# Optimization experiments

Hardware: AMD Instinct MI355X
Metric: run time of the kernel (lower is better)

## Reference

```python
import jax, jax.numpy as jnp
import numpy as np

CHUNK = 32  # chunk_size in _delta_rule_chunkwise

def _l2norm(x, eps=1e-6):
    return x * jax.lax.rsqrt(jnp.sum(x * x, axis=-1, keepdims=True) + eps)

def setup_inputs() -> dict:
    key = jax.random.key(0)
    kq, kk, kv, kb = jax.random.split(key, 4)
    b, h, L, dk, dv = 2, 8, 4096, 128, 128
    return {
        "q": jax.random.normal(kq, (b, h, L, dk), jnp.float32),
        "k": jax.random.normal(kk, (b, h, L, dk), jnp.float32),
        "v": jax.random.normal(kv, (b, h, L, dv), jnp.float32),
        "beta": jax.random.uniform(kb, (b, h, L), jnp.float32),  # sigmoid(b_proj) in (0,1)
    }

def _delta_rule_chunkwise(q, k, v, beta, chunk_size=CHUNK):
    b, h, L, dk = q.shape
    dv = v.shape[-1]
    c = chunk_size
    pad = (-L) % c
    if pad:
        q = jnp.pad(q, ((0, 0), (0, 0), (0, pad), (0, 0)))
        k = jnp.pad(k, ((0, 0), (0, 0), (0, pad), (0, 0)))
        v = jnp.pad(v, ((0, 0), (0, 0), (0, pad), (0, 0)))
        beta = jnp.pad(beta, ((0, 0), (0, 0), (0, pad)))
    n = (L + pad) // c
    q = _l2norm(q)
    k = _l2norm(k)
    v = v * beta[..., None]
    k_beta = k * beta[..., None]
    # [b,h,n,c,d]
    resh = lambda t: t.reshape(b, h, n, c, t.shape[-1])
    q, k, v, k_beta = map(resh, (q, k, v, k_beta))
    # strictly-lower-triangular -(k_beta k^T)
    lower = jnp.tril(jnp.ones((c, c), bool), -1)
    att = -(k_beta @ jnp.swapaxes(k, -1, -2)) * lower
    # forward substitution: invert (I - A) for strictly lower A (unrolled, c=32 static)
    for i in range(1, c):
        upd = jnp.einsum('...j,...jm->...m', att[..., i, :], att[..., :, :i])
        att = att.at[..., i, :i].add(upd)
    att = att + jnp.eye(c, dtype=att.dtype)
    att = att.astype(jnp.bfloat16).astype(q.dtype)  # matches .to(torch.bfloat16)
    u = att @ v         # [b,h,n,c,dv]
    w = att @ k_beta    # [b,h,n,c,dk]
    future = jnp.triu(jnp.ones((c, c), bool), 1)
    S0 = jnp.zeros((b, h, dk, dv), q.dtype)

    def step(S, inp):
        q_i, k_i, u_i, w_i = inp  # [b,h,c,d]
        att_local = jnp.where(future, 0.0, q_i @ jnp.swapaxes(k_i, -1, -2))
        u_new = u_i - w_i @ S
        o_i = q_i @ S + att_local @ u_new
        S_new = S + jnp.swapaxes(k_i, -1, -2) @ u_new
        return S_new, o_i

    xs = tuple(jnp.moveaxis(t, 2, 0) for t in (q, k, u, w))  # scan over chunks
    S, o = jax.lax.scan(step, S0, xs)
    o = jnp.moveaxis(o, 0, 2).reshape(b, h, n * c, dv)[:, :, :L]
    return o, S

def reference(q, k, v, beta):
    return _delta_rule_chunkwise(q, k, v, beta)
```

## Files before the change

kernel.cpp:

```cpp
#include <hip/hip_runtime.h>
#include <hip/hip_bf16.h>


#define B 2
#define H 8
#define LSEQ 4096
#define DK 128
#define DV 128
#define C 32
#define NCHUNK (LSEQ / C)
#define BH (B * H)
#define NBLK (BH * NCHUNK)

typedef _Float16 f16x8 __attribute__((ext_vector_type(8)));
typedef float f32x4 __attribute__((ext_vector_type(4)));

union U4H8 { uint4 u; f16x8 h; };

__device__ inline unsigned short f2h(float f) {
    _Float16 h = (_Float16)f;
    unsigned short u;
    __builtin_memcpy(&u, &h, 2);
    return u;
}
__device__ inline float h2f(unsigned int v) {
    unsigned short s = (unsigned short)v;
    _Float16 h;
    __builtin_memcpy(&h, &s, 2);
    return (float)h;
}
__device__ inline unsigned int pack2(float a, float b) {
    return (unsigned int)f2h(a) | ((unsigned int)f2h(b) << 16);
}
__device__ inline float dot4(float4 a, float4 b) {
    return a.x * b.x + a.y * b.y + a.z * b.z + a.w * b.w;
}
__device__ inline float bf16r(float x) {
    return __bfloat162float(__float2bfloat16(x));
}
__device__ inline uint2 pk4(float v0, float v1, float v2, float v3) {
    uint2 p; p.x = pack2(v0, v1); p.y = pack2(v2, v3); return p;
}

#define S40 40
#define S136 136

__global__ __launch_bounds__(64) void phase2_kernel(
    const float* __restrict__ qg, const float* __restrict__ kg,
    const float* __restrict__ vg, const float* __restrict__ betag,
    uint4* __restrict__ wnegf, uint4* __restrict__ qnf,
    uint4* __restrict__ ktf, uint4* __restrict__ atf,
    uint2* __restrict__ uf)
{
    __shared__ alignas(16) _Float16 sA [32 * S40];
    __shared__ alignas(16) _Float16 sAT[32 * S40];
    __shared__ alignas(16) _Float16 sTT[32 * S40];
    __shared__ alignas(16) _Float16 sTB[32 * S40];
    __shared__ alignas(16) _Float16 sW [32 * S136];
    __shared__ alignas(16) float sbetaL[32];
    __shared__ alignas(16) float skscL[32];

    const int l = threadIdx.x;
    const int lm = l & 15, qd = l >> 4;
    const int blk = blockIdx.x;
    const long tb = (long)blk * C * DK;
    const f32x4 z4 = {0.f, 0.f, 0.f, 0.f};

    if (l < 32) sbetaL[l] = betag[(long)blk * C + l];

    U4H8 qF[8], kF[8];
    float ssq[2] = {0.f, 0.f}, ssk[2] = {0.f, 0.f};
    #pragma unroll
    for (int mt = 0; mt < 2; mt++) {
        #pragma unroll
        for (int kt = 0; kt < 4; kt++) {
            const float* qp = qg + tb + (long)(mt * 16 + lm) * DK + kt * 32 + qd * 8;
            const float* kp = kg + tb + (long)(mt * 16 + lm) * DK + kt * 32 + qd * 8;
            float4 a0 = *(const float4*)qp, a1 = *(const float4*)(qp + 4);
            float4 b0 = *(const float4*)kp, b1 = *(const float4*)(kp + 4);
            ssq[mt] += dot4(a0, a0) + dot4(a1, a1);
            ssk[mt] += dot4(b0, b0) + dot4(b1, b1);
            U4H8 x;
            x.u.x = pack2(a0.x, a0.y); x.u.y = pack2(a0.z, a0.w);
            x.u.z = pack2(a1.x, a1.y); x.u.w = pack2(a1.z, a1.w);
            qF[mt * 4 + kt] = x;
            U4H8 y;
            y.u.x = pack2(b0.x, b0.y); y.u.y = pack2(b0.z, b0.w);
            y.u.z = pack2(b1.x, b1.y); y.u.w = pack2(b1.z, b1.w);
            kF[mt * 4 + kt] = y;
        }
    }
    float qsc[2], ksc[2];
    #pragma unroll
    for (int mt = 0; mt < 2; mt++) {
        float s = ssq[mt];
        s += __shfl_xor(s, 16, 64);
        s += __shfl_xor(s, 32, 64);
        qsc[mt] = rsqrtf(s + 1e-6f);
        float t = ssk[mt];
        t += __shfl_xor(t, 16, 64);
        t += __shfl_xor(t, 32, 64);
        ksc[mt] = rsqrtf(t + 1e-6f);
    }
    if (qd == 0) { skscL[lm] = ksc[0]; skscL[16 + lm] = ksc[1]; }

    f32x4 alT[3] = {z4, z4, z4};
    #pragma unroll
    for (int kt = 0; kt < 4; kt++) {
        alT[0] = __builtin_amdgcn_mfma_f32_16x16x32_f16(kF[kt].h,     qF[kt].h,     alT[0], 0, 0, 0);
        alT[1] = __builtin_amdgcn_mfma_f32_16x16x32_f16(kF[kt].h,     qF[4 + kt].h, alT[1], 0, 0, 0);
        alT[2] = __builtin_amdgcn_mfma_f32_16x16x32_f16(kF[4 + kt].h, qF[4 + kt].h, alT[2], 0, 0, 0);
    }
    #pragma unroll
    for (int mt = 0; mt < 2; mt++) {
        _Float16 qs = (_Float16)qsc[mt];
        #pragma unroll
        for (int kt = 0; kt < 4; kt++) {
            U4H8 x;
            x.h = qF[mt * 4 + kt].h * qs;
            qnf[((long)blk * 8 + mt * 4 + kt) * 64 + l] = x.u;
        }
    }
    f32x4 rw[4] = {z4, z4, z4, z4};
    #pragma unroll
    for (int kt = 0; kt < 4; kt++) {
        rw[0] = __builtin_amdgcn_mfma_f32_16x16x32_f16(kF[kt].h,     kF[kt].h,     rw[0], 0, 0, 0);
        rw[1] = __builtin_amdgcn_mfma_f32_16x16x32_f16(kF[kt].h,     kF[4 + kt].h, rw[1], 0, 0, 0);
        rw[2] = __builtin_amdgcn_mfma_f32_16x16x32_f16(kF[4 + kt].h, kF[kt].h,     rw[2], 0, 0, 0);
        rw[3] = __builtin_amdgcn_mfma_f32_16x16x32_f16(kF[4 + kt].h, kF[4 + kt].h, rw[3], 0, 0, 0);
    }

    float4 b4[2], ks4[2];
    b4[0]  = *(const float4*)&sbetaL[qd * 4];      b4[1]  = *(const float4*)&sbetaL[16 + qd * 4];
    ks4[0] = *(const float4*)&skscL[qd * 4];       ks4[1] = *(const float4*)&skscL[16 + qd * 4];
    const float bcol0 = sbetaL[lm], bcol1 = sbetaL[16 + lm];
    const float bA4[2] = {(&b4[0].x)[0], 0.f}; (void)bA4;

    {
        *(uint2*)&sTB[lm * S40 + 16 + qd * 4] = (uint2){0u, 0u};
        float v[4];
        #pragma unroll
        for (int r = 0; r < 4; r++) {
            int c = qd * 4 + r;
            v[r] = (c <= lm) ? (qsc[0] * (&ks4[0].x)[r] * alT[0][r]) : 0.f;
        }
        *(uint2*)&sTB[lm * S40 + qd * 4] = pk4(v[0], v[1], v[2], v[3]);
        #pragma unroll
        for (int r = 0; r < 4; r++) v[r] = qsc[1] * (&ks4[0].x)[r] * alT[1][r];
        *(uint2*)&sTB[(16 + lm) * S40 + qd * 4] = pk4(v[0], v[1], v[2], v[3]);
        #pragma unroll
        for (int r = 0; r < 4; r++) {
            int c = qd * 4 + r;
            v[r] = (c <= lm) ? (qsc[1] * (&ks4[1].x)[r] * alT[2][r]) : 0.f;
        }
        *(uint2*)&sTB[(16 + lm) * S40 + 16 + qd * 4] = pk4(v[0], v[1], v[2], v[3]);
    }
    #pragma unroll
    for (int f = 0; f < 2; f++) {
        uint4 x = *(const uint4*)&sTB[(f * 16 + lm) * S40 + qd * 8];
        atf[((long)blk * 2 + f) * 64 + l] = x;
    }

    {
        float v[4];
        *(uint2*)&sA [lm * S40 + 16 + qd * 4]        = (uint2){0u, 0u};
        *(uint2*)&sAT[(16 + lm) * S40 + qd * 4]      = (uint2){0u, 0u};
        *(uint2*)&sTT[(16 + lm) * S40 + qd * 4]      = (uint2){0u, 0u};
        #pragma unroll
        for (int r = 0; r < 4; r++) {
            int c = qd * 4 + r;
            v[r] = (c < lm) ? (-bcol0 * ksc[0] * (&ks4[0].x)[r] * rw[0][r]) : 0.f;
        }
        *(uint2*)&sA[lm * S40 + qd * 4] = pk4(v[0], v[1], v[2], v[3]);
        #pragma unroll
        for (int r = 0; r < 4; r++) v[r] = -bcol1 * ksc[1] * (&ks4[0].x)[r] * rw[1][r];
        *(uint2*)&sA[(16 + lm) * S40 + qd * 4] = pk4(v[0], v[1], v[2], v[3]);
        #pragma unroll
        for (int r = 0; r < 4; r++) {
            int c = qd * 4 + r;
            v[r] = (c < lm) ? (-bcol1 * ksc[1] * (&ks4[1].x)[r] * rw[3][r]) : 0.f;
        }
        *(uint2*)&sA[(16 + lm) * S40 + 16 + qd * 4] = pk4(v[0], v[1], v[2], v[3]);
        #pragma unroll
        for (int r = 0; r < 4; r++) {
            int c = qd * 4 + r;
            v[r] = (c > lm) ? (-(&b4[0].x)[r] * (&ks4[0].x)[r] * ksc[0] * rw[0][r]) : 0.f;
        }
        *(uint2*)&sAT[lm * S40 + qd * 4] = pk4(v[0], v[1], v[2], v[3]);
        #pragma unroll
        for (int r = 0; r < 4; r++) v[r] = -(&b4[1].x)[r] * (&ks4[1].x)[r] * ksc[0] * rw[2][r];
        *(uint2*)&sAT[lm * S40 + 16 + qd * 4] = pk4(v[0], v[1], v[2], v[3]);
        #pragma unroll
        for (int r = 0; r < 4; r++) {
            int c = qd * 4 + r;
            v[r] = (c > lm) ? (-(&b4[1].x)[r] * (&ks4[1].x)[r] * ksc[1] * rw[3][r]) : 0.f;
        }
        *(uint2*)&sAT[(16 + lm) * S40 + 16 + qd * 4] = pk4(v[0], v[1], v[2], v[3]);
        #pragma unroll
        for (int r = 0; r < 4; r++) {
            int c = qd * 4 + r;
            v[r] = (c > lm) ? (-(&b4[0].x)[r] * (&ks4[0].x)[r] * ksc[0] * rw[0][r])
                            : ((c == lm) ? 1.0f : 0.f);
        }
        *(uint2*)&sTT[lm * S40 + qd * 4] = pk4(v[0], v[1], v[2], v[3]);
        #pragma unroll
        for (int r = 0; r < 4; r++) v[r] = -(&b4[1].x)[r] * (&ks4[1].x)[r] * ksc[0] * rw[2][r];
        *(uint2*)&sTT[lm * S40 + 16 + qd * 4] = pk4(v[0], v[1], v[2], v[3]);
        #pragma unroll
        for (int r = 0; r < 4; r++) {
            int c = qd * 4 + r;
            v[r] = (c > lm) ? (-(&b4[1].x)[r] * (&ks4[1].x)[r] * ksc[1] * rw[3][r])
                            : ((c == lm) ? 1.0f : 0.f);
        }
        *(uint2*)&sTT[(16 + lm) * S40 + 16 + qd * 4] = pk4(v[0], v[1], v[2], v[3]);
    }
    f32x4 Tc[3], TTc[3];
    #pragma unroll
    for (int r = 0; r < 4; r++) {
        int rr = qd * 4 + r;
        Tc[0][r] = (lm < rr) ? (-(&b4[0].x)[r] * (&ks4[0].x)[r] * ksc[0] * rw[0][r])
                             : ((lm == rr) ? 1.0f : 0.f);
        Tc[1][r] = -(&b4[1].x)[r] * (&ks4[1].x)[r] * ksc[0] * rw[2][r];
        Tc[2][r] = (lm < rr) ? (-(&b4[1].x)[r] * (&ks4[1].x)[r] * ksc[1] * rw[3][r])
                             : ((lm == rr) ? 1.0f : 0.f);
        TTc[0][r] = (rr < lm) ? (-bcol0 * ksc[0] * (&ks4[0].x)[r] * rw[0][r])
                              : ((rr == lm) ? 1.0f : 0.f);
        TTc[1][r] = -bcol1 * ksc[1] * (&ks4[0].x)[r] * rw[1][r];
        TTc[2][r] = (rr < lm) ? (-bcol1 * ksc[1] * (&ks4[1].x)[r] * rw[3][r])
                              : ((rr == lm) ? 1.0f : 0.f);
    }

    #pragma unroll
    for (int p = 0; p < 4; p++) {
        U4H8 AF[2], ATF[2], TTF[2];
        AF[0].u  = *(const uint4*)&sA [lm * S40 + qd * 8];
        AF[1].u  = *(const uint4*)&sA [(16 + lm) * S40 + qd * 8];
        ATF[0].u = *(const uint4*)&sAT[lm * S40 + qd * 8];
        ATF[1].u = *(const uint4*)&sAT[(16 + lm) * S40 + qd * 8];
        TTF[0].u = *(const uint4*)&sTT[lm * S40 + qd * 8];
        TTF[1].u = *(const uint4*)&sTT[(16 + lm) * S40 + qd * 8];

        f32x4 A2_00 = __builtin_amdgcn_mfma_f32_16x16x32_f16(AF[0].h, ATF[0].h, z4, 0, 0, 0);
        f32x4 A2_10 = __builtin_amdgcn_mfma_f32_16x16x32_f16(AF[1].h, ATF[0].h, z4, 0, 0, 0);
        f32x4 A2_11 = __builtin_amdgcn_mfma_f32_16x16x32_f16(AF[1].h, ATF[1].h, z4, 0, 0, 0);
        f32x4 A2T_00 = __builtin_amdgcn_mfma_f32_16x16x32_f16(ATF[0].h, AF[0].h, z4, 0, 0, 0);
        f32x4 A2T_01 = __builtin_amdgcn_mfma_f32_16x16x32_f16(ATF[0].h, AF[1].h, z4, 0, 0, 0);
        f32x4 A2T_11 = __builtin_amdgcn_mfma_f32_16x16x32_f16(ATF[1].h, AF[1].h, z4, 0, 0, 0);

        {
            float v[4];
            #pragma unroll
            for (int r = 0; r < 4; r++) { int c = qd * 4 + r; v[r] = (c < lm) ? A2T_00[r] : 0.f; }
            *(uint2*)&sA[lm * S40 + qd * 4] = pk4(v[0], v[1], v[2], v[3]);
            *(uint2*)&sA[(16 + lm) * S40 + qd * 4] = pk4(A2T_01[0], A2T_01[1], A2T_01[2], A2T_01[3]);
            #pragma unroll
            for (int r = 0; r < 4; r++) { int c = qd * 4 + r; v[r] = (c < lm) ? A2T_11[r] : 0.f; }
            *(uint2*)&sA[(16 + lm) * S40 + 16 + qd * 4] = pk4(v[0], v[1], v[2], v[3]);
        }
        if (p < 3) {
            float v[4];
            #pragma unroll
            for (int r = 0; r < 4; r++) { int c = qd * 4 + r; v[r] = (c > lm) ? A2_00[r] : 0.f; }
            *(uint2*)&sAT[lm * S40 + qd * 4] = pk4(v[0], v[1], v[2], v[3]);
            *(uint2*)&sAT[lm * S40 + 16 + qd * 4] = pk4(A2_10[0], A2_10[1], A2_10[2], A2_10[3]);
            #pragma unroll
            for (int r = 0; r < 4; r++) { int c = qd * 4 + r; v[r] = (c > lm) ? A2_11[r] : 0.f; }
            *(uint2*)&sAT[(16 + lm) * S40 + 16 + qd * 4] = pk4(v[0], v[1], v[2], v[3]);
        }
        U4H8 AnF[2];
        AnF[0].u = *(const uint4*)&sA[lm * S40 + qd * 8];
        AnF[1].u = *(const uint4*)&sA[(16 + lm) * S40 + qd * 8];
        Tc[0]  = __builtin_amdgcn_mfma_f32_16x16x32_f16(AnF[0].h, TTF[0].h, Tc[0], 0, 0, 0);
        Tc[1]  = __builtin_amdgcn_mfma_f32_16x16x32_f16(AnF[1].h, TTF[0].h, Tc[1], 0, 0, 0);
        Tc[2]  = __builtin_amdgcn_mfma_f32_16x16x32_f16(AnF[1].h, TTF[1].h, Tc[2], 0, 0, 0);
        TTc[0] = __builtin_amdgcn_mfma_f32_16x16x32_f16(TTF[0].h, AnF[0].h, TTc[0], 0, 0, 0);
        TTc[1] = __builtin_amdgcn_mfma_f32_16x16x32_f16(TTF[0].h, AnF[1].h, TTc[1], 0, 0, 0);
        TTc[2] = __builtin_amdgcn_mfma_f32_16x16x32_f16(TTF[1].h, AnF[1].h, TTc[2], 0, 0, 0);
        if (p < 3) {
            *(uint2*)&sTT[lm * S40 + qd * 4]             = pk4(Tc[0][0], Tc[0][1], Tc[0][2], Tc[0][3]);
            *(uint2*)&sTT[lm * S40 + 16 + qd * 4]        = pk4(Tc[1][0], Tc[1][1], Tc[1][2], Tc[1][3]);
            *(uint2*)&sTT[(16 + lm) * S40 + 16 + qd * 4] = pk4(Tc[2][0], Tc[2][1], Tc[2][2], Tc[2][3]);
        }
    }

    {
        *(uint2*)&sTB[lm * S40 + 16 + qd * 4] = (uint2){0u, 0u};
        float v[4];
        #pragma unroll
        for (int r = 0; r < 4; r++) v[r] = bf16r(TTc[0][r]) * (&b4[0].x)[r];
        *(uint2*)&sTB[lm * S40 + qd * 4] = pk4(v[0], v[1], v[2], v[3]);
        #pragma unroll
        for (int r = 0; r < 4; r++) v[r] = bf16r(TTc[1][r]) * (&b4[0].x)[r];
        *(uint2*)&sTB[(16 + lm) * S40 + qd * 4] = pk4(v[0], v[1], v[2], v[3]);
        #pragma unroll
        for (int r = 0; r < 4; r++) v[r] = bf16r(TTc[2][r]) * (&b4[1].x)[r];
        *(uint2*)&sTB[(16 + lm) * S40 + 16 + qd * 4] = pk4(v[0], v[1], v[2], v[3]);
    }
    U4H8 TbF[2];
    TbF[0].u = *(const uint4*)&sTB[lm * S40 + qd * 8];
    TbF[1].u = *(const uint4*)&sTB[(16 + lm) * S40 + qd * 8];

    float kscj[8];
    #pragma unroll
    for (int j = 0; j < 8; j++) kscj[j] = skscL[qd * 8 + j];
    #pragma unroll
    for (int nt = 0; nt < 8; nt++) {
        U4H8 bV, bK;
        #pragma unroll
        for (int j = 0; j < 8; j++) {
            const long ro = tb + (long)(qd * 8 + j) * DK + nt * 16 + lm;
            bV.h[j] = (_Float16)vg[ro];
            bK.h[j] = (_Float16)(kg[ro] * kscj[j]);
        }
        ktf[((long)blk * 8 + nt) * 64 + l] = bK.u;
        f32x4 u0 = __builtin_amdgcn_mfma_f32_16x16x32_f16(TbF[0].h, bV.h, z4, 0, 0, 0);
        f32x4 u1 = __builtin_amdgcn_mfma_f32_16x16x32_f16(TbF[1].h, bV.h, z4, 0, 0, 0);
        uf[(((long)blk * 2 + 0) * 8 + nt) * 64 + l] = pk4(u0[0], u0[1], u0[2], u0[3]);
        uf[(((long)blk * 2 + 1) * 8 + nt) * 64 + l] = pk4(u1[0], u1[1], u1[2], u1[3]);
        f32x4 w0 = __builtin_amdgcn_mfma_f32_16x16x32_f16(TbF[0].h, bK.h, z4, 0, 0, 0);
        f32x4 w1 = __builtin_amdgcn_mfma_f32_16x16x32_f16(TbF[1].h, bK.h, z4, 0, 0, 0);
        #pragma unroll
        for (int r = 0; r < 4; r++) {
            sW[(qd * 4 + r) * S136 + nt * 16 + lm]        = (_Float16)(-w0[r]);
            sW[(16 + qd * 4 + r) * S136 + nt * 16 + lm]   = (_Float16)(-w1[r]);
        }
    }
    #pragma unroll
    for (int mt2 = 0; mt2 < 2; mt2++) {
        #pragma unroll
        for (int kt = 0; kt < 4; kt++) {
            uint4 x = *(const uint4*)&sW[(mt2 * 16 + lm) * S136 + kt * 32 + qd * 8];
            wnegf[((long)blk * 8 + mt2 * 4 + kt) * 64 + l] = x;
        }
    }
}

struct Frags {
    uint4 aW[2][4];
    uint4 aQ[2][4];
    uint4 aK[8];
    uint4 aAt[2];
    uint2 aU[2];
};

__global__ __launch_bounds__(64, 1) void phase3_kernel(
    const uint4* __restrict__ wnegf, const uint4* __restrict__ qnf,
    const uint4* __restrict__ ktf, const uint4* __restrict__ atf,
    const uint2* __restrict__ uf,
    float* __restrict__ o_out, float* __restrict__ S_out)
{
    __shared__ alignas(16) _Float16 S16[16 * 16 * 8];
    __shared__ alignas(16) _Float16 U16[4 * 16 * 8];

    const int l = threadIdx.x;
    const int lm = l & 15, quad = l >> 4;
    const int bh = blockIdx.x & 15;
    const int w = blockIdx.x >> 4;
    const int dv = w * 16 + lm;

    f32x4 accS[8];
    #pragma unroll
    for (int mt = 0; mt < 8; mt++) accS[mt] = (f32x4){0.f, 0.f, 0.f, 0.f};

    auto loadf = [&](Frags& f, int nc) {
        long blk = (long)bh * NCHUNK + nc;
        #pragma unroll
        for (int mt2 = 0; mt2 < 2; mt2++) {
            #pragma unroll
            for (int kt = 0; kt < 4; kt++) {
                f.aW[mt2][kt] = wnegf[(blk * 8 + mt2 * 4 + kt) * 64 + l];
                f.aQ[mt2][kt] = qnf[(blk * 8 + mt2 * 4 + kt) * 64 + l];
            }
            f.aAt[mt2] = atf[(blk * 2 + mt2) * 64 + l];
            f.aU[mt2] = uf[((blk * 2 + mt2) * 8 + w) * 64 + l];
        }
        #pragma unroll
        for (int mt = 0; mt < 8; mt++) f.aK[mt] = ktf[(blk * 8 + mt) * 64 + l];
    };

    auto compute = [&](const Frags& f, int nc) {
        #pragma unroll
        for (int mt = 0; mt < 8; mt++) {
            int g = 2 * mt + (quad >> 1);
            int sub = (quad & 1) * 4;
            *(uint2*)&S16[(g * 16 + lm) * 8 + sub] =
                pk4(accS[mt][0], accS[mt][1], accS[mt][2], accS[mt][3]);
        }
        f32x4 accU[2], accO[2];
        #pragma unroll
        for (int mt2 = 0; mt2 < 2; mt2++) {
            accU[mt2][0] = h2f(f.aU[mt2].x & 0xffffu);
            accU[mt2][1] = h2f(f.aU[mt2].x >> 16);
            accU[mt2][2] = h2f(f.aU[mt2].y & 0xffffu);
            accU[mt2][3] = h2f(f.aU[mt2].y >> 16);
            accO[mt2] = (f32x4){0.f, 0.f, 0.f, 0.f};
        }
        #pragma unroll
        for (int kt = 0; kt < 4; kt++) {
            U4H8 bs;
            bs.u = *(const uint4*)&S16[((kt * 4 + quad) * 16 + lm) * 8];
            #pragma unroll
            for (int mt2 = 0; mt2 < 2; mt2++) {
                U4H8 aw, aq;
                aw.u = f.aW[mt2][kt];
                aq.u = f.aQ[mt2][kt];
                accU[mt2] = __builtin_amdgcn_mfma_f32_16x16x32_f16(aw.h, bs.h, accU[mt2], 0, 0, 0);
                accO[mt2] = __builtin_amdgcn_mfma_f32_16x16x32_f16(aq.h, bs.h, accO[mt2], 0, 0, 0);
            }
        }
        #pragma unroll
        for (int mt2 = 0; mt2 < 2; mt2++) {
            int g = 2 * mt2 + (quad >> 1);
            int sub = (quad & 1) * 4;
            *(uint2*)&U16[(g * 16 + lm) * 8 + sub] =
                pk4(accU[mt2][0], accU[mt2][1], accU[mt2][2], accU[mt2][3]);
        }
        U4H8 bu;
        bu.u = *(const uint4*)&U16[(quad * 16 + lm) * 8];
        const long ob = ((long)bh * LSEQ + (long)nc * C) * DV;
        #pragma unroll
        for (int mt2 = 0; mt2 < 2; mt2++) {
            U4H8 aa;
            aa.u = f.aAt[mt2];
            accO[mt2] = __builtin_amdgcn_mfma_f32_16x16x32_f16(aa.h, bu.h, accO[mt2], 0, 0, 0);
            #pragma unroll
            for (int r = 0; r < 4; r++)
                o_out[ob + (long)(mt2 * 16 + quad * 4 + r) * DV + dv] = accO[mt2][r];
        }
        #pragma unroll
        for (int mt = 0; mt < 8; mt++) {
            U4H8 ak;
            ak.u = f.aK[mt];
            accS[mt] = __builtin_amdgcn_mfma_f32_16x16x32_f16(ak.h, bu.h, accS[mt], 0, 0, 0);
        }
    };

    Frags fA, fB;
    loadf(fA, 0);
    #pragma unroll 1
    for (int nc = 0; nc < NCHUNK; nc += 2) {
        loadf(fB, (nc + 1 < NCHUNK - 1) ? nc + 1 : NCHUNK - 1);
        compute(fA, nc);
        loadf(fA, (nc + 2 < NCHUNK - 1) ? nc + 2 : NCHUNK - 1);
        compute(fB, nc + 1);
    }
    #pragma unroll
    for (int mt = 0; mt < 8; mt++) {
        #pragma unroll
        for (int r = 0; r < 4; r++)
            S_out[(long)bh * (DK * DV) + (long)(mt * 16 + quad * 4 + r) * DV + dv] = accS[mt][r];
    }
}

extern "C" void kernel_launch(void* const* d_in, const int* in_sizes, int n_in,
                              void* d_out, int out_size, void* d_ws, size_t ws_size,
                              hipStream_t stream) {
    const float* q    = (const float*)d_in[0];
    const float* k    = (const float*)d_in[1];
    const float* v    = (const float*)d_in[2];
    const float* beta = (const float*)d_in[3];

    float* o = (float*)d_out;
    float* S = o + (long)BH * LSEQ * DV;

    const size_t nwq = (size_t)NBLK * 8 * 64;
    uint4* wnegf = (uint4*)d_ws;
    uint4* qnf = wnegf + nwq;
    uint4* ktf = qnf + nwq;
    uint4* atf = ktf + nwq;
    uint2* uf  = (uint2*)(atf + (size_t)NBLK * 2 * 64);

    phase2_kernel<<<NBLK, 64, 0, stream>>>(q, k, v, beta, wnegf, qnf, ktf, atf, uf);
    phase3_kernel<<<BH * 8, 64, 0, stream>>>(wnegf, qnf, ktf, atf, uf, o, S);
}
```

Before: 235.3 us.

## Parallelize chunk recurrence via group-wise affine state composition

Replaces the serial 128-chunk scan (128 blocks) with a three-stage scheme. First, each group of 8 chunks computes its local state contribution from zero and its transition matrix, one 16-column slice per block. Second, a short 16-step scan composes the group states. Third, the groups replay their chunks in parallel from the composed start states to produce outputs. This exposes far more parallelism than the 128-block serial kernel, at the cost of extra MFMA work, extra fp16 intermediate traffic, two more launches, and rounding from the fp16 transition products.

```diff
diff --git a/kernel.cpp b/kernel.cpp
--- a/kernel.cpp
+++ b/kernel.cpp
@@ -11,6 +11,8 @@
 #define NCHUNK (LSEQ / C)
 #define BH (B * H)
 #define NBLK (BH * NCHUNK)
+#define NG 16
+#define GSZ 8
 
 typedef _Float16 f16x8 __attribute__((ext_vector_type(8)));
 typedef float f32x4 __attribute__((ext_vector_type(4)));
@@ -40,6 +42,12 @@
 }
 __device__ inline uint2 pk4(float v0, float v1, float v2, float v3) {
     uint2 p; p.x = pack2(v0, v1); p.y = pack2(v2, v3); return p;
+}
+__device__ inline f32x4 up4(uint2 p) {
+    f32x4 v;
+    v[0] = h2f(p.x & 0xffffu); v[1] = h2f(p.x >> 16);
+    v[2] = h2f(p.y & 0xffffu); v[3] = h2f(p.y >> 16);
+    return v;
 }
 
 #define S40 40
@@ -134,7 +142,6 @@
     b4[0]  = *(const float4*)&sbetaL[qd * 4];      b4[1]  = *(const float4*)&sbetaL[16 + qd * 4];
     ks4[0] = *(const float4*)&skscL[qd * 4];       ks4[1] = *(const float4*)&skscL[16 + qd * 4];
     const float bcol0 = sbetaL[lm], bcol1 = sbetaL[16 + lm];
-    const float bA4[2] = {(&b4[0].x)[0], 0.f}; (void)bA4;
 
     {
         *(uint2*)&sTB[lm * S40 + 16 + qd * 4] = (uint2){0u, 0u};
@@ -335,6 +342,206 @@
     }
 }
 
+__global__ __launch_bounds__(64, 2) void phase3a_kernel(
+    const uint4* __restrict__ wnegf, const uint4* __restrict__ ktf,
+    const uint2* __restrict__ uf,
+    uint4* __restrict__ Pf, uint2* __restrict__ Qgf)
+{
+    __shared__ alignas(16) _Float16 S16[16 * 16 * 8];
+    __shared__ alignas(16) _Float16 U16[4 * 16 * 8];
+    __shared__ alignas(16) _Float16 PT[128 * 16];
+
+    const int l = threadIdx.x;
+    const int lm = l & 15, quad = l >> 4;
+    const int idx = blockIdx.x;
+    const int mode = idx >> 11;
+    const int r2 = idx & 2047;
+    const int bh = r2 >> 7;
+    const int grp = (r2 >> 3) & 15;
+    const int w = r2 & 7;
+    const f32x4 z4 = {0.f, 0.f, 0.f, 0.f};
+
+    if (mode && grp == 0) return;
+
+    f32x4 accS[8];
+    #pragma unroll
+    for (int mt = 0; mt < 8; mt++) {
+        #pragma unroll
+        for (int r = 0; r < 4; r++)
+            accS[mt][r] = (mode && mt == w && quad * 4 + r == lm) ? 1.f : 0.f;
+    }
+
+    struct FragA { uint4 aW[2][4]; uint4 aK[8]; uint2 aU[2]; };
+    FragA fA, fB;
+
+    auto loadf = [&](FragA& f, int t) {
+        const long blk = (long)bh * NCHUNK + grp * GSZ + t;
+        #pragma unroll
+        for (int mt2 = 0; mt2 < 2; mt2++)
+            #pragma unroll
+            for (int kt = 0; kt < 4; kt++)
+                f.aW[mt2][kt] = wnegf[(blk * 8 + mt2 * 4 + kt) * 64 + l];
+        #pragma unroll
+        for (int mt = 0; mt < 8; mt++) f.aK[mt] = ktf[(blk * 8 + mt) * 64 + l];
+        if (!mode) {
+            #pragma unroll
+            for (int mt2 = 0; mt2 < 2; mt2++)
+                f.aU[mt2] = uf[((blk * 2 + mt2) * 8 + w) * 64 + l];
+        }
+    };
+
+    auto compute = [&](const FragA& f) {
+        #pragma unroll
+        for (int mt = 0; mt < 8; mt++) {
+            int g = 2 * mt + (quad >> 1);
+            int sub = (quad & 1) * 4;
+            *(uint2*)&S16[(g * 16 + lm) * 8 + sub] =
+                pk4(accS[mt][0], accS[mt][1], accS[mt][2], accS[mt][3]);
+        }
+        f32x4 accU[2];
+        #pragma unroll
+        for (int mt2 = 0; mt2 < 2; mt2++)
+            accU[mt2] = mode ? z4 : up4(f.aU[mt2]);
+        #pragma unroll
+        for (int kt = 0; kt < 4; kt++) {
+            U4H8 bs;
+            bs.u = *(const uint4*)&S16[((kt * 4 + quad) * 16 + lm) * 8];
+            #pragma unroll
+            for (int mt2 = 0; mt2 < 2; mt2++) {
+                U4H8 aw; aw.u = f.aW[mt2][kt];
+                accU[mt2] = __builtin_amdgcn_mfma_f32_16x16x32_f16(aw.h, bs.h, accU[mt2], 0, 0, 0);
+            }
+        }
+        #pragma unroll
+        for (int mt2 = 0; mt2 < 2; mt2++) {
+            int g = 2 * mt2 + (quad >> 1);
+            int sub = (quad & 1) * 4;
+            *(uint2*)&U16[(g * 16 + lm) * 8 + sub] =
+                pk4(accU[mt2][0], accU[mt2][1], accU[mt2][2], accU[mt2][3]);
+        }
+        U4H8 bu;
+        bu.u = *(const uint4*)&U16[(quad * 16 + lm) * 8];
+        #pragma unroll
+        for (int mt = 0; mt < 8; mt++) {
+            U4H8 ak; ak.u = f.aK[mt];
+            accS[mt] = __builtin_amdgcn_mfma_f32_16x16x32_f16(ak.h, bu.h, accS[mt], 0, 0, 0);
+        }
+    };
+
+    loadf(fA, 0);
+    #pragma unroll 1
+    for (int t = 0; t < GSZ; t += 2) {
+        loadf(fB, t + 1);
+        compute(fA);
+        if (t + 2 < GSZ) loadf(fA, t + 2);
+        compute(fB);
+    }
+
+    if (!mode) {
+        const long qb = (((long)(bh * NG + grp)) * 8 + w) * 8 * 64;
+        #pragma unroll
+        for (int mt = 0; mt < 8; mt++)
+            Qgf[qb + mt * 64 + l] = pk4(accS[mt][0], accS[mt][1], accS[mt][2], accS[mt][3]);
+    } else {
+        #pragma unroll
+        for (int mt = 0; mt < 8; mt++)
+            #pragma unroll
+            for (int r = 0; r < 4; r++)
+                PT[(mt * 16 + quad * 4 + r) * 16 + lm] = (_Float16)accS[mt][r];
+        const int tl = ((w & 1) << 5) | (l & 31);
+        const int half = l >> 5;
+        const long pb = ((long)(bh * NG + grp)) * 8;
+        #pragma unroll
+        for (int i = 0; i < 4; i++) {
+            int mt = half * 4 + i;
+            uint4 x = *(const uint4*)&PT[(mt * 16 + (tl & 15)) * 16 + ((tl >> 4) & 1) * 8];
+            Pf[((pb + mt) * 4 + (w >> 1)) * 64 + tl] = x;
+        }
+    }
+}
+
+__global__ __launch_bounds__(64, 1) void phase3b_kernel(
+    const uint4* __restrict__ Pf, const uint2* __restrict__ Qgf,
+    uint2* __restrict__ Sjf, float* __restrict__ S_out)
+{
+    __shared__ alignas(16) _Float16 S16[16 * 16 * 8];
+
+    const int l = threadIdx.x;
+    const int lm = l & 15, quad = l >> 4;
+    const int bh = blockIdx.x >> 3;
+    const int w = blockIdx.x & 7;
+
+    f32x4 accS[8];
+    #pragma unroll
+    for (int mt = 0; mt < 8; mt++) accS[mt] = (f32x4){0.f, 0.f, 0.f, 0.f};
+
+    uint2 Q0[8], Q1[8];
+    uint4 P0[8][4], P1[8][4];
+
+    auto loadQ = [&](uint2 (&Q)[8], int j) {
+        const long b = (((long)(bh * NG + j)) * 8 + w) * 8 * 64;
+        #pragma unroll
+        for (int mt = 0; mt < 8; mt++) Q[mt] = Qgf[b + mt * 64 + l];
+    };
+    auto loadP = [&](uint4 (&P)[8][4], int j) {
+        const long b = ((long)(bh * NG + j)) * 8;
+        #pragma unroll
+        for (int mt = 0; mt < 8; mt++)
+            #pragma unroll
+            for (int kt = 0; kt < 4; kt++)
+                P[mt][kt] = Pf[((b + mt) * 4 + kt) * 64 + l];
+    };
+    auto computeB = [&](int j, const uint2 (&Q)[8], const uint4 (&P)[8][4]) {
+        f32x4 ns[8];
+        #pragma unroll
+        for (int mt = 0; mt < 8; mt++) ns[mt] = up4(Q[mt]);
+        if (j) {
+            #pragma unroll
+            for (int mt = 0; mt < 8; mt++) {
+                int g = 2 * mt + (quad >> 1);
+                int sub = (quad & 1) * 4;
+                *(uint2*)&S16[(g * 16 + lm) * 8 + sub] =
+                    pk4(accS[mt][0], accS[mt][1], accS[mt][2], accS[mt][3]);
+            }
+            #pragma unroll
+            for (int kt = 0; kt < 4; kt++) {
+                U4H8 bs;
+                bs.u = *(const uint4*)&S16[((kt * 4 + quad) * 16 + lm) * 8];
+                #pragma unroll
+                for (int mt = 0; mt < 8; mt++) {
+                    U4H8 ap; ap.u = P[mt][kt];
+                    ns[mt] = __builtin_amdgcn_mfma_f32_16x16x32_f16(ap.h, bs.h, ns[mt], 0, 0, 0);
+                }
+            }
+        }
+        #pragma unroll
+        for (int mt = 0; mt < 8; mt++) accS[mt] = ns[mt];
+        if (j < 15) {
+            const long sb = (((long)(bh * 16 + (j + 1))) * 8 + w) * 8 * 64;
+            #pragma unroll
+            for (int mt = 0; mt < 8; mt++)
+                Sjf[sb + mt * 64 + l] = pk4(ns[mt][0], ns[mt][1], ns[mt][2], ns[mt][3]);
+        } else {
+            #pragma unroll
+            for (int mt = 0; mt < 8; mt++)
+                #pragma unroll
+                for (int r = 0; r < 4; r++)
+                    S_out[(long)bh * (DK * DV) + (long)(mt * 16 + quad * 4 + r) * DV + w * 16 + lm] = ns[mt][r];
+        }
+    };
+
+    loadQ(Q0, 0);
+    loadP(P1, 1);
+    #pragma unroll 1
+    for (int j = 0; j < 16; j += 2) {
+        loadQ(Q1, j + 1);
+        computeB(j, Q0, P0);
+        if (j + 2 < 16) { loadP(P0, j + 2); loadQ(Q0, j + 2); }
+        computeB(j + 1, Q1, P1);
+        if (j + 3 < 16) loadP(P1, j + 3);
+    }
+}
+
 struct Frags {
     uint4 aW[2][4];
     uint4 aQ[2][4];
@@ -343,27 +550,35 @@
     uint2 aU[2];
 };
 
-__global__ __launch_bounds__(64, 1) void phase3_kernel(
+__global__ __launch_bounds__(64, 1) void phase3c_kernel(
     const uint4* __restrict__ wnegf, const uint4* __restrict__ qnf,
     const uint4* __restrict__ ktf, const uint4* __restrict__ atf,
-    const uint2* __restrict__ uf,
-    float* __restrict__ o_out, float* __restrict__ S_out)
+    const uint2* __restrict__ uf, const uint2* __restrict__ Sjf,
+    float* __restrict__ o_out)
 {
     __shared__ alignas(16) _Float16 S16[16 * 16 * 8];
     __shared__ alignas(16) _Float16 U16[4 * 16 * 8];
 
     const int l = threadIdx.x;
     const int lm = l & 15, quad = l >> 4;
-    const int bh = blockIdx.x & 15;
-    const int w = blockIdx.x >> 4;
+    const int b = blockIdx.x;
+    const int bh = b >> 7;
+    const int grp = (b >> 3) & 15;
+    const int w = b & 7;
     const int dv = w * 16 + lm;
 
     f32x4 accS[8];
-    #pragma unroll
-    for (int mt = 0; mt < 8; mt++) accS[mt] = (f32x4){0.f, 0.f, 0.f, 0.f};
-
-    auto loadf = [&](Frags& f, int nc) {
-        long blk = (long)bh * NCHUNK + nc;
+    if (grp == 0) {
+        #pragma unroll
+        for (int mt = 0; mt < 8; mt++) accS[mt] = (f32x4){0.f, 0.f, 0.f, 0.f};
+    } else {
+        const long sb = (((long)(bh * 16 + grp)) * 8 + w) * 8 * 64;
+        #pragma unroll
+        for (int mt = 0; mt < 8; mt++) accS[mt] = up4(Sjf[sb + mt * 64 + l]);
+    }
+
+    auto loadf = [&](Frags& f, int t) {
+        const long blk = (long)bh * NCHUNK + grp * GSZ + t;
         #pragma unroll
         for (int mt2 = 0; mt2 < 2; mt2++) {
             #pragma unroll
@@ -378,7 +593,7 @@
         for (int mt = 0; mt < 8; mt++) f.aK[mt] = ktf[(blk * 8 + mt) * 64 + l];
     };
 
-    auto compute = [&](const Frags& f, int nc) {
+    auto compute = [&](const Frags& f, int t) {
         #pragma unroll
         for (int mt = 0; mt < 8; mt++) {
             int g = 2 * mt + (quad >> 1);
@@ -389,10 +604,7 @@
         f32x4 accU[2], accO[2];
         #pragma unroll
         for (int mt2 = 0; mt2 < 2; mt2++) {
-            accU[mt2][0] = h2f(f.aU[mt2].x & 0xffffu);
-            accU[mt2][1] = h2f(f.aU[mt2].x >> 16);
-            accU[mt2][2] = h2f(f.aU[mt2].y & 0xffffu);
-            accU[mt2][3] = h2f(f.aU[mt2].y >> 16);
+            accU[mt2] = up4(f.aU[mt2]);
             accO[mt2] = (f32x4){0.f, 0.f, 0.f, 0.f};
         }
         #pragma unroll
@@ -417,7 +629,7 @@
         }
         U4H8 bu;
         bu.u = *(const uint4*)&U16[(quad * 16 + lm) * 8];
-        const long ob = ((long)bh * LSEQ + (long)nc * C) * DV;
+        const long ob = ((long)bh * LSEQ + (long)(grp * GSZ + t) * C) * DV;
         #pragma unroll
         for (int mt2 = 0; mt2 < 2; mt2++) {
             U4H8 aa;
@@ -438,17 +650,11 @@
     Frags fA, fB;
     loadf(fA, 0);
     #pragma unroll 1
-    for (int nc = 0; nc < NCHUNK; nc += 2) {
-        loadf(fB, (nc + 1 < NCHUNK - 1) ? nc + 1 : NCHUNK - 1);
-        compute(fA, nc);
-        loadf(fA, (nc + 2 < NCHUNK - 1) ? nc + 2 : NCHUNK - 1);
-        compute(fB, nc + 1);
-    }
-    #pragma unroll
-    for (int mt = 0; mt < 8; mt++) {
-        #pragma unroll
-        for (int r = 0; r < 4; r++)
-            S_out[(long)bh * (DK * DV) + (long)(mt * 16 + quad * 4 + r) * DV + dv] = accS[mt][r];
+    for (int t = 0; t < GSZ; t += 2) {
+        loadf(fB, t + 1);
+        compute(fA, t);
+        if (t + 2 < GSZ) loadf(fA, t + 2);
+        compute(fB, t + 1);
     }
 }
 
@@ -469,7 +675,12 @@
     uint4* ktf = qnf + nwq;
     uint4* atf = ktf + nwq;
     uint2* uf  = (uint2*)(atf + (size_t)NBLK * 2 * 64);
+    uint4* Pf  = (uint4*)(uf + (size_t)NBLK * 16 * 64);
+    uint2* Qgf = (uint2*)(Pf + (size_t)BH * NG * 8 * 4 * 64);
+    uint2* Sjf = Qgf + (size_t)BH * NG * 8 * 8 * 64;
 
     phase2_kernel<<<NBLK, 64, 0, stream>>>(q, k, v, beta, wnegf, qnf, ktf, atf, uf);
-    phase3_kernel<<<BH * 8, 64, 0, stream>>>(wnegf, qnf, ktf, atf, uf, o, S);
-}
+    phase3a_kernel<<<BH * NG * 8 * 2, 64, 0, stream>>>(wnegf, ktf, uf, Pf, Qgf);
+    phase3b_kernel<<<BH * 8, 64, 0, stream>>>(Pf, Qgf, Sjf, S);
+    phase3c_kernel<<<BH * NG * 8, 64, 0, stream>>>(wnegf, qnf, ktf, atf, uf, Sjf, o);
+}
```

Measured after the change: 317.2 us. +34.8%, slower.
